# Kernel tuning notes

Hardware: AMD Instinct MI355X
Metric: run time of the kernel (lower is better)

Reference implementation:

```python
import jax, jax.numpy as jnp
import numpy as np

B, T, C, H = 8, 2048, 1024, 64  # batch, seq, n_embed, head_size


def setup_inputs() -> dict:
    key = jax.random.key(0)
    ks = jax.random.split(key, 6)
    k = jax.random.normal(ks[0], (B, T, C), dtype=jnp.float32)
    q = jax.random.normal(ks[1], (B, T, C), dtype=jnp.float32)
    v = jax.random.normal(ks[2], (B, T, C), dtype=jnp.float32)
    mask = jnp.ones((B, T), dtype=jnp.int32)  # key-padding mask (1 = keep)
    # nn.Linear(n_embed, head_size, bias=False) weights: [head_size, n_embed]
    s = 1.0 / np.sqrt(C)
    Wk = jax.random.uniform(ks[3], (H, C), jnp.float32, -s, s)
    Wq = jax.random.uniform(ks[4], (H, C), jnp.float32, -s, s)
    Wv = jax.random.uniform(ks[5], (H, C), jnp.float32, -s, s)
    return {"k": k, "q": q, "v": v, "mask": mask, "Wk": Wk, "Wq": Wq, "Wv": Wv}


def reference(k, q, v, mask, Wk, Wq, Wv):
    Tq = q.shape[1]
    kh = jnp.einsum('btc,hc->bth', k, Wk)   # [B,T,H]
    qh = jnp.einsum('btc,hc->bth', q, Wq)   # [B,T,H]
    vh = jnp.einsum('btc,hc->bth', v, Wv)   # [B,T,H]
    scale = kh.shape[-1] ** -0.5
    wei = jnp.einsum('bqh,bkh->bqk', qh, kh) * scale  # [B,T,T]
    # causal (tril) mask
    tril = jnp.tril(jnp.ones((Tq, Tq), dtype=bool))
    neg_inf = jnp.finfo(wei.dtype).min
    wei = jnp.where(tril[None, :, :], wei, neg_inf)
    # key-padding mask: mask [B,T] -> broadcast over query rows
    wei = jnp.where(mask[:, None, :] != 0, wei, neg_inf)
    wei = jax.nn.softmax(wei, axis=-1)
    # dropout p=0.0 (eval) -> identity
    out = jnp.einsum('bqk,bkh->bqh', wei, vh)  # [B,T,H]
    return out
```

## Files before the change

### kernel.cpp

```cpp
#include <hip/hip_runtime.h>
#include <hip/hip_bf16.h>
#include <math.h>

#define Bn 8
#define Tn 2048
#define Cn 1024
#define Hn 64
#define BTHb ((size_t)Bn * Tn * Hn)

typedef __attribute__((ext_vector_type(8))) short bf16x8;
typedef __attribute__((ext_vector_type(4))) float f32x4;

static __device__ __forceinline__ unsigned short bf16rne(float f) {
    union { float f; unsigned u; } x; x.f = f;
    return (unsigned short)((x.u + 0x7FFFu + ((x.u >> 16) & 1u)) >> 16);
}

__global__ __launch_bounds__(256) void proj_kernel(
    const float* __restrict__ k, const float* __restrict__ q,
    const float* __restrict__ v,
    const float* __restrict__ Wk, const float* __restrict__ Wq,
    const float* __restrict__ Wv,
    unsigned short* __restrict__ ws)
{
    const int which = blockIdx.y;
    const float* X = (which == 0) ? k : (which == 1) ? q : v;
    const float* W = (which == 0) ? Wk : (which == 1) ? Wq : Wv;
    unsigned short* O = ws + (size_t)which * BTHb;

    __shared__ unsigned short Xs[64][72];
    __shared__ unsigned short Wt[64][72];

    const int tid  = threadIdx.x;
    const int wave = __builtin_amdgcn_readfirstlane(tid >> 6);
    const int lane = tid & 63;
    const int m    = lane & 15;
    const int quad = lane >> 4;
    const int row0 = blockIdx.x * 64;

    const int srow = tid >> 4;
    const int sc4  = tid & 15;

    f32x4 acc[4];
#pragma unroll
    for (int t = 0; t < 4; ++t) acc[t] = (f32x4){0.f, 0.f, 0.f, 0.f};

    float4 xr[4], wr[4];
#pragma unroll
    for (int u = 0; u < 4; ++u) {
        const int row = srow + 16 * u;
        xr[u] = *(const float4*)(X + (size_t)(row0 + row) * Cn + sc4 * 4);
        wr[u] = *(const float4*)(W + (size_t)row * Cn + sc4 * 4);
    }

    for (int ct = 0; ct < 16; ++ct) {
        __syncthreads();
#pragma unroll
        for (int u = 0; u < 4; ++u) {
            const int row = srow + 16 * u;
            ushort4 xb, wb;
            xb.x = bf16rne(xr[u].x); xb.y = bf16rne(xr[u].y);
            xb.z = bf16rne(xr[u].z); xb.w = bf16rne(xr[u].w);
            wb.x = bf16rne(wr[u].x); wb.y = bf16rne(wr[u].y);
            wb.z = bf16rne(wr[u].z); wb.w = bf16rne(wr[u].w);
            *(ushort4*)&Xs[row][sc4 * 4] = xb;
            *(ushort4*)&Wt[row][sc4 * 4] = wb;
        }
        __syncthreads();

        if (ct < 15) {
#pragma unroll
            for (int u = 0; u < 4; ++u) {
                const int row = srow + 16 * u;
                xr[u] = *(const float4*)(X + (size_t)(row0 + row) * Cn
                                           + (ct + 1) * 64 + sc4 * 4);
                wr[u] = *(const float4*)(W + (size_t)row * Cn
                                           + (ct + 1) * 64 + sc4 * 4);
            }
        }

#pragma unroll
        for (int kc = 0; kc < 64; kc += 32) {
            const bf16x8 a = *(const bf16x8*)&Xs[wave * 16 + m][kc + quad * 8];
#pragma unroll
            for (int ht = 0; ht < 4; ++ht) {
                const bf16x8 bfr =
                    *(const bf16x8*)&Wt[ht * 16 + m][kc + quad * 8];
                acc[ht] = __builtin_amdgcn_mfma_f32_16x16x32_bf16(
                    a, bfr, acc[ht], 0, 0, 0);
            }
        }
    }

#pragma unroll
    for (int ht = 0; ht < 4; ++ht)
#pragma unroll
        for (int r = 0; r < 4; ++r)
            O[(size_t)(row0 + wave * 16 + quad * 4 + r) * Hn + ht * 16 + m] =
                bf16rne(acc[ht][r]);
}

__global__ __launch_bounds__(256) void attn_kernel(
    const unsigned short* __restrict__ ws,
    const int* __restrict__ mask,
    float* __restrict__ out)
{
    const unsigned short* kh = ws;
    const unsigned short* qh = ws + BTHb;
    const unsigned short* vh = ws + 2 * BTHb;

    const int b   = blockIdx.y;
    const int qt  = blockIdx.x;
    const int tid = threadIdx.x;
    const int wave = __builtin_amdgcn_readfirstlane(tid >> 6);
    const int lane = tid & 63;
    const int ln   = lane & 15;
    const int quad = lane >> 4;

    __shared__ unsigned short Ks[64][72];
    __shared__ unsigned short Vt[64][72];
    __shared__ unsigned short Ps[64][72];
    __shared__ int Msk[64];

    const int wrb = qt * 64 + wave * 16;

    bf16x8 qa[2];
#pragma unroll
    for (int kc = 0; kc < 2; ++kc)
        qa[kc] = *(const bf16x8*)(qh + ((size_t)b * Tn + wrb + ln) * Hn
                                     + kc * 32 + quad * 8);

    f32x4 oacc[4];
#pragma unroll
    for (int t = 0; t < 4; ++t) oacc[t] = (f32x4){0.f, 0.f, 0.f, 0.f};
    float mrow[4] = {-1e30f, -1e30f, -1e30f, -1e30f};
    float lrow[4] = {0.f, 0.f, 0.f, 0.f};

    const int krow = tid >> 2, kseg = tid & 3;
    const int vcol = tid & 63, vseg = tid >> 6;

    uint4 kreg[2], vreg[2];
    int mreg = 0;
    {
        const unsigned short* kp =
            kh + ((size_t)b * Tn + krow) * Hn + kseg * 16;
        kreg[0] = *(const uint4*)kp;
        kreg[1] = *(const uint4*)(kp + 8);
        const unsigned short* vp =
            vh + ((size_t)b * Tn + vcol) * Hn + vseg * 16;
        vreg[0] = *(const uint4*)vp;
        vreg[1] = *(const uint4*)(vp + 8);
        if (tid < 64) mreg = mask[(size_t)b * Tn + tid];
    }

    for (int j = 0; j <= qt; ++j) {
        __syncthreads();
        *(uint4*)&Ks[krow][kseg * 16]     = kreg[0];
        *(uint4*)&Ks[krow][kseg * 16 + 8] = kreg[1];
        {
            const unsigned short* vs = (const unsigned short*)vreg;
#pragma unroll
            for (int jj = 0; jj < 16; ++jj)
                Vt[vseg * 16 + jj][vcol] = vs[jj];
        }
        if (tid < 64) Msk[tid] = mreg;
        __syncthreads();

        if (j < qt) {
            const unsigned short* kp =
                kh + ((size_t)b * Tn + (j + 1) * 64 + krow) * Hn + kseg * 16;
            kreg[0] = *(const uint4*)kp;
            kreg[1] = *(const uint4*)(kp + 8);
            const unsigned short* vp =
                vh + ((size_t)b * Tn + (j + 1) * 64 + vcol) * Hn + vseg * 16;
            vreg[0] = *(const uint4*)vp;
            vreg[1] = *(const uint4*)(vp + 8);
            if (tid < 64) mreg = mask[(size_t)b * Tn + (j + 1) * 64 + tid];
        }

        f32x4 sacc[4];
#pragma unroll
        for (int t = 0; t < 4; ++t) sacc[t] = (f32x4){0.f, 0.f, 0.f, 0.f};
#pragma unroll
        for (int kc = 0; kc < 2; ++kc) {
#pragma unroll
            for (int nt = 0; nt < 4; ++nt) {
                const bf16x8 kb =
                    *(const bf16x8*)&Ks[nt * 16 + ln][kc * 32 + quad * 8];
                sacc[nt] = __builtin_amdgcn_mfma_f32_16x16x32_bf16(
                    qa[kc], kb, sacc[nt], 0, 0, 0);
            }
        }

        const bool fullv = (j < qt);
        float pv[4][4];
        float mt[4] = {-1e30f, -1e30f, -1e30f, -1e30f};
#pragma unroll
        for (int nt = 0; nt < 4; ++nt) {
            const bool mk = (Msk[nt * 16 + ln] != 0);
            const int kpos = j * 64 + nt * 16 + ln;
#pragma unroll
            for (int r = 0; r < 4; ++r) {
                float s = sacc[nt][r] * 0.125f;
                const bool valid =
                    mk && (fullv || kpos <= wrb + quad * 4 + r);
                s = valid ? s : -1e30f;
                pv[nt][r] = s;
                mt[r] = fmaxf(mt[r], s);
            }
        }
#pragma unroll
        for (int r = 0; r < 4; ++r) {
            mt[r] = fmaxf(mt[r], __shfl_xor(mt[r], 1));
            mt[r] = fmaxf(mt[r], __shfl_xor(mt[r], 2));
            mt[r] = fmaxf(mt[r], __shfl_xor(mt[r], 4));
            mt[r] = fmaxf(mt[r], __shfl_xor(mt[r], 8));
        }
        float alpha[4], rsum[4];
#pragma unroll
        for (int r = 0; r < 4; ++r) {
            const float mn = fmaxf(mrow[r], mt[r]);
            alpha[r] = __expf(mrow[r] - mn);
            mrow[r] = mn;
            rsum[r] = 0.f;
        }
#pragma unroll
        for (int nt = 0; nt < 4; ++nt)
#pragma unroll
            for (int r = 0; r < 4; ++r) {
                const float p = (pv[nt][r] <= -1e29f)
                                    ? 0.f
                                    : __expf(pv[nt][r] - mrow[r]);
                pv[nt][r] = p;
                rsum[r] += p;
            }
#pragma unroll
        for (int r = 0; r < 4; ++r) {
            rsum[r] += __shfl_xor(rsum[r], 1);
            rsum[r] += __shfl_xor(rsum[r], 2);
            rsum[r] += __shfl_xor(rsum[r], 4);
            rsum[r] += __shfl_xor(rsum[r], 8);
            lrow[r] = lrow[r] * alpha[r] + rsum[r];
        }
#pragma unroll
        for (int nt = 0; nt < 4; ++nt)
#pragma unroll
            for (int r = 0; r < 4; ++r) oacc[nt][r] *= alpha[r];

#pragma unroll
        for (int nt = 0; nt < 4; ++nt)
#pragma unroll
            for (int r = 0; r < 4; ++r)
                Ps[wave * 16 + quad * 4 + r][nt * 16 + ln] =
                    bf16rne(pv[nt][r]);
        asm volatile("s_waitcnt lgkmcnt(0)" ::: "memory");

#pragma unroll
        for (int kc = 0; kc < 2; ++kc) {
            const bf16x8 pa =
                *(const bf16x8*)&Ps[wave * 16 + ln][kc * 32 + quad * 8];
#pragma unroll
            for (int nt = 0; nt < 4; ++nt) {
                const bf16x8 vb =
                    *(const bf16x8*)&Vt[nt * 16 + ln][kc * 32 + quad * 8];
                oacc[nt] = __builtin_amdgcn_mfma_f32_16x16x32_bf16(
                    pa, vb, oacc[nt], 0, 0, 0);
            }
        }
    }

#pragma unroll
    for (int r = 0; r < 4; ++r) {
        const float inv = 1.0f / lrow[r];
        const size_t rowoff = ((size_t)b * Tn + wrb + quad * 4 + r) * Hn;
#pragma unroll
        for (int nt = 0; nt < 4; ++nt)
            out[rowoff + nt * 16 + ln] = oacc[nt][r] * inv;
    }
}

extern "C" void kernel_launch(void* const* d_in, const int* in_sizes, int n_in,
                              void* d_out, int out_size, void* d_ws, size_t ws_size,
                              hipStream_t stream)
{
    const float* k    = (const float*)d_in[0];
    const float* q    = (const float*)d_in[1];
    const float* v    = (const float*)d_in[2];
    const int*   mask = (const int*)d_in[3];
    const float* Wk   = (const float*)d_in[4];
    const float* Wq   = (const float*)d_in[5];
    const float* Wv   = (const float*)d_in[6];
    float* out = (float*)d_out;
    unsigned short* ws = (unsigned short*)d_ws;

    dim3 pb(256), pg(Bn * Tn / 64, 3);
    proj_kernel<<<pg, pb, 0, stream>>>(k, q, v, Wk, Wq, Wv, ws);

    dim3 ab(256), ag(Tn / 64, Bn);
    attn_kernel<<<ag, ab, 0, stream>>>(ws, mask, out);
}
```

Before: 279.7 us.

## Pre-convert weights to bf16 and load X fragments directly into registers

A small new kernel converts the three weight matrices to bf16 once per call and stores them in workspace. The projection kernel then stages only the bf16 weights in LDS, using a 128-wide K tile. Each lane loads its own X fragment straight from global memory into registers and converts it to bf16 there, with no LDS round trip. This removes the per-block weight conversion and the X shared-memory staging, and halves the number of K-loop barriers. The cost is one extra kernel launch and uncoalesced-ish per-lane X loads of 32 bytes each.

After: 298.0 us. +6.5%, slower.

```diff
diff --git a/kernel.cpp b/kernel.cpp
--- a/kernel.cpp
+++ b/kernel.cpp
@@ -7,6 +7,7 @@
 #define Cn 1024
 #define Hn 64
 #define BTHb ((size_t)Bn * Tn * Hn)
+#define WELEMS ((size_t)Hn * Cn)
 
 typedef __attribute__((ext_vector_type(8))) short bf16x8;
 typedef __attribute__((ext_vector_type(4))) float f32x4;
@@ -16,78 +17,109 @@
     return (unsigned short)((x.u + 0x7FFFu + ((x.u >> 16) & 1u)) >> 16);
 }
 
+__global__ __launch_bounds__(256) void wconv_kernel(
+    const float* __restrict__ Wk, const float* __restrict__ Wq,
+    const float* __restrict__ Wv, unsigned short* __restrict__ dst)
+{
+    const int g = blockIdx.x * 256 + threadIdx.x;
+    const float* src = (g < 16384) ? Wk : (g < 32768) ? Wq : Wv;
+    const int local = g & 16383;
+    const float4 f = ((const float4*)src)[local];
+    ushort4 u;
+    u.x = bf16rne(f.x); u.y = bf16rne(f.y);
+    u.z = bf16rne(f.z); u.w = bf16rne(f.w);
+    ((ushort4*)dst)[g] = u;
+}
+
 __global__ __launch_bounds__(256) void proj_kernel(
     const float* __restrict__ k, const float* __restrict__ q,
     const float* __restrict__ v,
-    const float* __restrict__ Wk, const float* __restrict__ Wq,
-    const float* __restrict__ Wv,
     unsigned short* __restrict__ ws)
 {
     const int which = blockIdx.y;
     const float* X = (which == 0) ? k : (which == 1) ? q : v;
-    const float* W = (which == 0) ? Wk : (which == 1) ? Wq : Wv;
+    const unsigned short* Wsrc = ws + 3 * BTHb + (size_t)which * WELEMS;
     unsigned short* O = ws + (size_t)which * BTHb;
 
-    __shared__ unsigned short Xs[64][72];
-    __shared__ unsigned short Wt[64][72];
+    __shared__ unsigned short Wt[64][136];
 
     const int tid  = threadIdx.x;
     const int wave = __builtin_amdgcn_readfirstlane(tid >> 6);
     const int lane = tid & 63;
-    const int m    = lane & 15;
+    const int ln   = lane & 15;
     const int quad = lane >> 4;
     const int row0 = blockIdx.x * 64;
 
-    const int srow = tid >> 4;
-    const int sc4  = tid & 15;
+    const int wrow = tid >> 2;
+    const int wseg = tid & 3;
+
+    const float* Xrow = X + (size_t)(row0 + wave * 16 + ln) * Cn + quad * 8;
 
     f32x4 acc[4];
 #pragma unroll
     for (int t = 0; t < 4; ++t) acc[t] = (f32x4){0.f, 0.f, 0.f, 0.f};
 
-    float4 xr[4], wr[4];
-#pragma unroll
-    for (int u = 0; u < 4; ++u) {
-        const int row = srow + 16 * u;
-        xr[u] = *(const float4*)(X + (size_t)(row0 + row) * Cn + sc4 * 4);
-        wr[u] = *(const float4*)(W + (size_t)row * Cn + sc4 * 4);
-    }
-
-    for (int ct = 0; ct < 16; ++ct) {
+    uint4  wreg[4];
+    float4 xr[8];
+
+    {
+        const uint4* wp =
+            (const uint4*)(Wsrc + (size_t)wrow * Cn + wseg * 32);
+#pragma unroll
+        for (int u = 0; u < 4; ++u) wreg[u] = wp[u];
+    }
+#pragma unroll
+    for (int kc = 0; kc < 4; ++kc) {
+        xr[2 * kc]     = *(const float4*)(Xrow + kc * 32);
+        xr[2 * kc + 1] = *(const float4*)(Xrow + kc * 32 + 4);
+    }
+
+    for (int ct = 0; ct < 8; ++ct) {
         __syncthreads();
-#pragma unroll
-        for (int u = 0; u < 4; ++u) {
-            const int row = srow + 16 * u;
-            ushort4 xb, wb;
-            xb.x = bf16rne(xr[u].x); xb.y = bf16rne(xr[u].y);
-            xb.z = bf16rne(xr[u].z); xb.w = bf16rne(xr[u].w);
-            wb.x = bf16rne(wr[u].x); wb.y = bf16rne(wr[u].y);
-            wb.z = bf16rne(wr[u].z); wb.w = bf16rne(wr[u].w);
-            *(ushort4*)&Xs[row][sc4 * 4] = xb;
-            *(ushort4*)&Wt[row][sc4 * 4] = wb;
+        {
+            uint4* wd = (uint4*)&Wt[wrow][wseg * 32];
+#pragma unroll
+            for (int u = 0; u < 4; ++u) wd[u] = wreg[u];
         }
         __syncthreads();
 
-        if (ct < 15) {
-#pragma unroll
-            for (int u = 0; u < 4; ++u) {
-                const int row = srow + 16 * u;
-                xr[u] = *(const float4*)(X + (size_t)(row0 + row) * Cn
-                                           + (ct + 1) * 64 + sc4 * 4);
-                wr[u] = *(const float4*)(W + (size_t)row * Cn
-                                           + (ct + 1) * 64 + sc4 * 4);
-            }
-        }
-
-#pragma unroll
-        for (int kc = 0; kc < 64; kc += 32) {
-            const bf16x8 a = *(const bf16x8*)&Xs[wave * 16 + m][kc + quad * 8];
+        if (ct < 7) {
+            const uint4* wp = (const uint4*)(Wsrc + (size_t)wrow * Cn
+                                             + (ct + 1) * 128 + wseg * 32);
+#pragma unroll
+            for (int u = 0; u < 4; ++u) wreg[u] = wp[u];
+        }
+
+        bf16x8 af[4];
+#pragma unroll
+        for (int kc = 0; kc < 4; ++kc) {
+            union { bf16x8 v; unsigned short s[8]; } u;
+            const float4 a = xr[2 * kc], b = xr[2 * kc + 1];
+            u.s[0] = bf16rne(a.x); u.s[1] = bf16rne(a.y);
+            u.s[2] = bf16rne(a.z); u.s[3] = bf16rne(a.w);
+            u.s[4] = bf16rne(b.x); u.s[5] = bf16rne(b.y);
+            u.s[6] = bf16rne(b.z); u.s[7] = bf16rne(b.w);
+            af[kc] = u.v;
+        }
+
+        if (ct < 7) {
+#pragma unroll
+            for (int kc = 0; kc < 4; ++kc) {
+                xr[2 * kc]     = *(const float4*)(Xrow + (ct + 1) * 128
+                                                  + kc * 32);
+                xr[2 * kc + 1] = *(const float4*)(Xrow + (ct + 1) * 128
+                                                  + kc * 32 + 4);
+            }
+        }
+
+#pragma unroll
+        for (int kc = 0; kc < 4; ++kc) {
 #pragma unroll
             for (int ht = 0; ht < 4; ++ht) {
                 const bf16x8 bfr =
-                    *(const bf16x8*)&Wt[ht * 16 + m][kc + quad * 8];
+                    *(const bf16x8*)&Wt[ht * 16 + ln][kc * 32 + quad * 8];
                 acc[ht] = __builtin_amdgcn_mfma_f32_16x16x32_bf16(
-                    a, bfr, acc[ht], 0, 0, 0);
+                    af[kc], bfr, acc[ht], 0, 0, 0);
             }
         }
     }
@@ -96,7 +128,7 @@
     for (int ht = 0; ht < 4; ++ht)
 #pragma unroll
         for (int r = 0; r < 4; ++r)
-            O[(size_t)(row0 + wave * 16 + quad * 4 + r) * Hn + ht * 16 + m] =
+            O[(size_t)(row0 + wave * 16 + quad * 4 + r) * Hn + ht * 16 + ln] =
                 bf16rne(acc[ht][r]);
 }
 
@@ -293,8 +325,11 @@
     float* out = (float*)d_out;
     unsigned short* ws = (unsigned short*)d_ws;
 
+    wconv_kernel<<<dim3(192), dim3(256), 0, stream>>>(Wk, Wq, Wv,
+                                                      ws + 3 * BTHb);
+
     dim3 pb(256), pg(Bn * Tn / 64, 3);
-    proj_kernel<<<pg, pb, 0, stream>>>(k, q, v, Wk, Wq, Wv, ws);
+    proj_kernel<<<pg, pb, 0, stream>>>(k, q, v, ws);
 
     dim3 ab(256), ag(Tn / 64, Bn);
     attn_kernel<<<ag, ab, 0, stream>>>(ws, mask, out);
```
